# Performance work log

Hardware: AMD Instinct MI355X
Metric: run time of the kernel (lower is better)

Reference implementation:

```python
import jax, jax.numpy as jnp
import numpy as np

B, T, D = 4, 4096, 1024
HD = 64              # head_dim
H = D // HD          # n_heads = 16
C = 64               # chunk_size (T % C == 0)


def setup_inputs() -> dict:
    key = jax.random.key(0)
    k1, k2, k3 = jax.random.split(key, 3)
    out = jax.random.normal(k1, (B, T, D), jnp.float32)
    # Linear(d_model, d_model, bias=False) weights, ~1/sqrt(D) scale
    W_write = jax.random.normal(k2, (D, D), jnp.float32) * 0.03
    W_read = jax.random.normal(k3, (D, D), jnp.float32) * 0.03
    decay = jnp.full((H,), 4.6, jnp.float32)                 # torch init value
    log_alpha = jnp.log(jnp.full((H,), 0.03, jnp.float32))   # memory_alpha=0.03
    return {"out": out, "W_write": W_write, "W_read": W_read,
            "decay": decay, "log_alpha": log_alpha}


def reference(out, W_write, W_read, decay, log_alpha):
    Bb, Tt, Dd = out.shape
    d, Hh, Cc = HD, D // HD, C
    out32 = out.astype(jnp.float32)
    gamma = jax.nn.sigmoid(decay)          # (H,)
    log_gamma = jnp.log(gamma)

    # projections and head split: (B, H, T, d)
    v = (out32 @ W_write.T).reshape(Bb, Tt, Hh, d).transpose(0, 2, 1, 3)
    rk = out32.reshape(Bb, Tt, Hh, d).transpose(0, 2, 1, 3)
    wk = jnp.pad(rk[:, :, :-1], ((0, 0), (0, 0), (1, 0), (0, 0)))  # shift right by 1

    BH = Bb * Hh
    gamma_bh = jnp.tile(gamma, Bb)          # (BH,) index b*H+h -> gamma[h]
    log_gamma_bh = jnp.tile(log_gamma, Bb)
    nC = Tt // Cc
    # (nC, BH, C, d) so lax.scan runs over chunks
    v_ch = v.reshape(BH, nC, Cc, d).transpose(1, 0, 2, 3)
    rk_ch = rk.reshape(BH, nC, Cc, d).transpose(1, 0, 2, 3)
    wk_ch = wk.reshape(BH, nC, Cc, d).transpose(1, 0, 2, 3)

    p = jnp.arange(Cc)
    diffs = jnp.clip(p[:, None] - 1 - p[None, :], 0)          # (C, C)
    causal = p[:, None] > p[None, :]
    # per-(b,h) intra-chunk decay mask (BH, C, C)
    M = jnp.exp(diffs[None].astype(jnp.float32) * log_gamma_bh[:, None, None]) * causal[None]
    g_p = gamma_bh[:, None] ** p[None, :].astype(jnp.float32)            # (BH, C)
    g_w = gamma_bh[:, None] ** (Cc - 1 - p)[None, :].astype(jnp.float32)  # (BH, C)
    g_C = gamma_bh ** Cc                                                  # (BH,)

    def scan_fn(W, chunk):
        rk_c, wk_c, v_c = chunk                                   # each (BH, C, d)
        inter = jnp.einsum('bij,bcj->bci', W, rk_c) * g_p[:, :, None]
        S = jnp.einsum('bcd,bkd->bck', rk_c, wk_c)                # (BH, C, C)
        intra = jnp.einsum('bck,bkd->bcd', S * M, v_c)
        W_new = g_C[:, None, None] * W + jnp.einsum('bci,bcj->bij', v_c * g_w[:, :, None], wk_c)
        return W_new, inter + intra

    W0 = jnp.zeros((BH, d, d), jnp.float32)
    _, reads = jax.lax.scan(scan_fn, W0, (rk_ch, wk_ch, v_ch))   # (nC, BH, C, d)
    reads = reads.transpose(1, 0, 2, 3).reshape(Bb, Hh, Tt, d)
    alpha = jnp.exp(log_alpha)[None, :, None, None]
    reads = (alpha * reads).transpose(0, 2, 1, 3).reshape(Bb, Tt, Dd)
    return out + (reads @ W_read.T).astype(out.dtype)
```

## Files before the change

kernel.cpp:

```cpp
#include <hip/hip_runtime.h>
#include <hip/hip_bf16.h>
#include <stdint.h>


typedef __bf16 bf16x8 __attribute__((ext_vector_type(8)));
typedef float f32x4 __attribute__((ext_vector_type(4)));

#define GAS __attribute__((address_space(1)))
#define LAS __attribute__((address_space(3)))

__device__ __forceinline__ unsigned short f2bf(float f) {
  unsigned u = __float_as_uint(f);
  u = (u + 0x7fffu + ((u >> 16) & 1u)) >> 16;
  return (unsigned short)u;
}
__device__ __forceinline__ float bf2f(unsigned short h) {
  return __uint_as_float(((unsigned)h) << 16);
}

__global__ __launch_bounds__(256) void cast_f32_to_bf16(
    const float* __restrict__ src, unsigned short* __restrict__ dst, int n8) {
  int i = blockIdx.x * 256 + threadIdx.x;
  if (i >= n8) return;
  const float4* s = (const float4*)src + (size_t)i * 2;
  float4 f0 = s[0], f1 = s[1];
  union { uint4 u4; unsigned short us[8]; } o;
  o.us[0] = f2bf(f0.x); o.us[1] = f2bf(f0.y); o.us[2] = f2bf(f0.z); o.us[3] = f2bf(f0.w);
  o.us[4] = f2bf(f1.x); o.us[5] = f2bf(f1.y); o.us[6] = f2bf(f1.z); o.us[7] = f2bf(f1.w);
  ((uint4*)dst)[i] = o.u4;
}

__device__ __forceinline__ void swizzle_bm_bn(int id, int& bm, int& bn) {
  int x = id & 7;
  int s = id >> 3;
  bn = s & 7;
  bm = ((s >> 3) << 3) | x;
}

__global__ __launch_bounds__(256, 4) void gemm_bt_bf16out(
    const unsigned short* __restrict__ A, const unsigned short* __restrict__ B,
    unsigned short* __restrict__ C, int M, int N, int K) {
  __shared__ unsigned short As[2][128 * 32];
  __shared__ unsigned short Bs[2][128 * 32];
  int tid = threadIdx.x;
  int l = tid & 63, w = tid >> 6;
  int bm, bn;
  swizzle_bm_bn(blockIdx.x, bm, bn);
  int wm = (w >> 1) * 64, wn = (w & 1) * 64;
  f32x4 acc[4][4];
#pragma unroll
  for (int mi = 0; mi < 4; mi++)
#pragma unroll
    for (int ni = 0; ni < 4; ni++) acc[mi][ni] = (f32x4){0.f, 0.f, 0.f, 0.f};
  const unsigned short* Ab = A + (size_t)bm * 128 * K;
  const unsigned short* Bb = B + (size_t)bn * 128 * K;
  int lr = l >> 2, lc = (l & 3) * 8;
  int lm = l & 15, q4 = l >> 4;
  const int nit = K >> 5;

#pragma unroll
  for (int q = 0; q < 2; q++) {
    int g = (w * 2 + q) * 16 + lr;
    __builtin_amdgcn_global_load_lds((GAS void*)(void*)(Ab + (size_t)g * K + lc),
                                     (LAS void*)(&As[0][(w * 2 + q) * 512]), 16, 0, 0);
    __builtin_amdgcn_global_load_lds((GAS void*)(void*)(Bb + (size_t)g * K + lc),
                                     (LAS void*)(&Bs[0][(w * 2 + q) * 512]), 16, 0, 0);
  }
  for (int it = 0; it < nit; it++) {
    __syncthreads();
    int buf = it & 1;
    if (it + 1 < nit) {
      int k0 = (it + 1) << 5;
#pragma unroll
      for (int q = 0; q < 2; q++) {
        int g = (w * 2 + q) * 16 + lr;
        __builtin_amdgcn_global_load_lds((GAS void*)(void*)(Ab + (size_t)g * K + k0 + lc),
                                         (LAS void*)(&As[buf ^ 1][(w * 2 + q) * 512]), 16, 0, 0);
        __builtin_amdgcn_global_load_lds((GAS void*)(void*)(Bb + (size_t)g * K + k0 + lc),
                                         (LAS void*)(&Bs[buf ^ 1][(w * 2 + q) * 512]), 16, 0, 0);
      }
    }
    bf16x8 a[4], b[4];
#pragma unroll
    for (int mi = 0; mi < 4; mi++) a[mi] = *(const bf16x8*)&As[buf][(wm + mi * 16 + lm) * 32 + q4 * 8];
#pragma unroll
    for (int ni = 0; ni < 4; ni++) b[ni] = *(const bf16x8*)&Bs[buf][(wn + ni * 16 + lm) * 32 + q4 * 8];
#pragma unroll
    for (int mi = 0; mi < 4; mi++)
#pragma unroll
      for (int ni = 0; ni < 4; ni++)
        acc[mi][ni] = __builtin_amdgcn_mfma_f32_16x16x32_bf16(a[mi], b[ni], acc[mi][ni], 0, 0, 0);
  }
#pragma unroll
  for (int mi = 0; mi < 4; mi++)
#pragma unroll
    for (int ni = 0; ni < 4; ni++) {
      int r0 = bm * 128 + wm + mi * 16 + q4 * 4;
      int col = bn * 128 + wn + ni * 16 + lm;
#pragma unroll
      for (int j = 0; j < 4; j++)
        C[(size_t)(r0 + j) * N + col] = f2bf(acc[mi][ni][j]);
    }
}

__global__ __launch_bounds__(256, 4) void gemm_bt_addout(
    const unsigned short* __restrict__ A, const unsigned short* __restrict__ B,
    const float* __restrict__ base, float* __restrict__ C, int M, int N, int K) {
  __shared__ unsigned short As[2][128 * 32];
  __shared__ unsigned short Bs[2][128 * 32];
  int tid = threadIdx.x;
  int l = tid & 63, w = tid >> 6;
  int bm, bn;
  swizzle_bm_bn(blockIdx.x, bm, bn);
  int wm = (w >> 1) * 64, wn = (w & 1) * 64;
  int lr = l >> 2, lc = (l & 3) * 8;
  int lm = l & 15, q4 = l >> 4;
  f32x4 acc[4][4];
#pragma unroll
  for (int mi = 0; mi < 4; mi++)
#pragma unroll
    for (int ni = 0; ni < 4; ni++) {
      int r0 = bm * 128 + wm + mi * 16 + q4 * 4;
      int col = bn * 128 + wn + ni * 16 + lm;
#pragma unroll
      for (int j = 0; j < 4; j++)
        acc[mi][ni][j] = base[(size_t)(r0 + j) * N + col];
    }
  const unsigned short* Ab = A + (size_t)bm * 128 * K;
  const unsigned short* Bb = B + (size_t)bn * 128 * K;
  const int nit = K >> 5;
#pragma unroll
  for (int q = 0; q < 2; q++) {
    int g = (w * 2 + q) * 16 + lr;
    __builtin_amdgcn_global_load_lds((GAS void*)(void*)(Ab + (size_t)g * K + lc),
                                     (LAS void*)(&As[0][(w * 2 + q) * 512]), 16, 0, 0);
    __builtin_amdgcn_global_load_lds((GAS void*)(void*)(Bb + (size_t)g * K + lc),
                                     (LAS void*)(&Bs[0][(w * 2 + q) * 512]), 16, 0, 0);
  }
  for (int it = 0; it < nit; it++) {
    __syncthreads();
    int buf = it & 1;
    if (it + 1 < nit) {
      int k0 = (it + 1) << 5;
#pragma unroll
      for (int q = 0; q < 2; q++) {
        int g = (w * 2 + q) * 16 + lr;
        __builtin_amdgcn_global_load_lds((GAS void*)(void*)(Ab + (size_t)g * K + k0 + lc),
                                         (LAS void*)(&As[buf ^ 1][(w * 2 + q) * 512]), 16, 0, 0);
        __builtin_amdgcn_global_load_lds((GAS void*)(void*)(Bb + (size_t)g * K + k0 + lc),
                                         (LAS void*)(&Bs[buf ^ 1][(w * 2 + q) * 512]), 16, 0, 0);
      }
    }
    bf16x8 a[4], b[4];
#pragma unroll
    for (int mi = 0; mi < 4; mi++) a[mi] = *(const bf16x8*)&As[buf][(wm + mi * 16 + lm) * 32 + q4 * 8];
#pragma unroll
    for (int ni = 0; ni < 4; ni++) b[ni] = *(const bf16x8*)&Bs[buf][(wn + ni * 16 + lm) * 32 + q4 * 8];
#pragma unroll
    for (int mi = 0; mi < 4; mi++)
#pragma unroll
      for (int ni = 0; ni < 4; ni++)
        acc[mi][ni] = __builtin_amdgcn_mfma_f32_16x16x32_bf16(a[mi], b[ni], acc[mi][ni], 0, 0, 0);
  }
#pragma unroll
  for (int mi = 0; mi < 4; mi++)
#pragma unroll
    for (int ni = 0; ni < 4; ni++) {
      int r0 = bm * 128 + wm + mi * 16 + q4 * 4;
      int col = bn * 128 + wn + ni * 16 + lm;
#pragma unroll
      for (int j = 0; j < 4; j++)
        C[(size_t)(r0 + j) * N + col] = acc[mi][ni][j];
    }
}

__global__ __launch_bounds__(256) void chunk_local(
    const unsigned short* __restrict__ rkg,
    const unsigned short* __restrict__ vg,
    const float* __restrict__ decay,
    unsigned short* __restrict__ intra_bf,
    unsigned short* __restrict__ U_bf) {
  int c = blockIdx.x, bh = blockIdx.y;
  int b = bh >> 4, h = bh & 15;
  int tid = threadIdx.x, l = tid & 63, w = tid >> 6;
  float gamma = 1.0f / (1.0f + __expf(-decay[h]));
  float lg = __logf(gamma);

  __shared__ unsigned short rk_s[64 * 72];
  __shared__ unsigned short wk_s[64 * 72];
  __shared__ unsigned short wkT_s[64 * 72];
  __shared__ unsigned short vT_s[64 * 72];
  __shared__ unsigned short S_s[64 * 72];

  const size_t rowbase = (((size_t)b * 4096 + (size_t)c * 64) * 1024) + h * 64;

#pragma unroll
  for (int r = 0; r < 2; r++) {
    int e = r * 256 + tid;
    int p = e >> 3, seg = e & 7;
    uint4 dr = *(const uint4*)(rkg + rowbase + (size_t)p * 1024 + seg * 8);
    *(uint4*)&rk_s[p * 72 + seg * 8] = dr;
    uint4 dv = *(const uint4*)(vg + rowbase + (size_t)p * 1024 + seg * 8);
    {
      unsigned uu[4] = {dv.x, dv.y, dv.z, dv.w};
#pragma unroll
      for (int qq = 0; qq < 4; qq++) {
        vT_s[(seg * 8 + qq * 2) * 72 + p] = (unsigned short)(uu[qq] & 0xffffu);
        vT_s[(seg * 8 + qq * 2 + 1) * 72 + p] = (unsigned short)(uu[qq] >> 16);
      }
    }
    int tg = c * 64 + p - 1;
    uint4 dw = make_uint4(0u, 0u, 0u, 0u);
    if (tg >= 0) dw = *(const uint4*)(rkg + ((size_t)b * 4096 + tg) * 1024 + h * 64 + seg * 8);
    *(uint4*)&wk_s[p * 72 + seg * 8] = dw;
    {
      unsigned uu[4] = {dw.x, dw.y, dw.z, dw.w};
#pragma unroll
      for (int qq = 0; qq < 4; qq++) {
        wkT_s[(seg * 8 + qq * 2) * 72 + p] = (unsigned short)(uu[qq] & 0xffffu);
        wkT_s[(seg * 8 + qq * 2 + 1) * 72 + p] = (unsigned short)(uu[qq] >> 16);
      }
    }
  }
  __syncthreads();

  int lm = l & 15, q4 = l >> 4;

  {
    bf16x8 a0 = *(const bf16x8*)&rk_s[(w * 16 + lm) * 72 + q4 * 8];
    bf16x8 a1 = *(const bf16x8*)&rk_s[(w * 16 + lm) * 72 + 32 + q4 * 8];
#pragma unroll
    for (int ni = 0; ni < 4; ni++) {
      bf16x8 b0 = *(const bf16x8*)&wk_s[(ni * 16 + lm) * 72 + q4 * 8];
      bf16x8 b1 = *(const bf16x8*)&wk_s[(ni * 16 + lm) * 72 + 32 + q4 * 8];
      f32x4 acc = {0.f, 0.f, 0.f, 0.f};
      acc = __builtin_amdgcn_mfma_f32_16x16x32_bf16(a0, b0, acc, 0, 0, 0);
      acc = __builtin_amdgcn_mfma_f32_16x16x32_bf16(a1, b1, acc, 0, 0, 0);
#pragma unroll
      for (int j = 0; j < 4; j++) {
        int p = w * 16 + q4 * 4 + j;
        int q = ni * 16 + lm;
        float m = (p > q) ? __expf(lg * (float)(p - 1 - q)) : 0.0f;
        S_s[p * 72 + q] = f2bf(acc[j] * m);
      }
    }
  }
  __syncthreads();

  {
    bf16x8 a0 = *(const bf16x8*)&S_s[(w * 16 + lm) * 72 + q4 * 8];
    bf16x8 a1 = *(const bf16x8*)&S_s[(w * 16 + lm) * 72 + 32 + q4 * 8];
#pragma unroll
    for (int ni = 0; ni < 4; ni++) {
      bf16x8 b0 = *(const bf16x8*)&vT_s[(ni * 16 + lm) * 72 + q4 * 8];
      bf16x8 b1 = *(const bf16x8*)&vT_s[(ni * 16 + lm) * 72 + 32 + q4 * 8];
      f32x4 acc = {0.f, 0.f, 0.f, 0.f};
      acc = __builtin_amdgcn_mfma_f32_16x16x32_bf16(a0, b0, acc, 0, 0, 0);
      acc = __builtin_amdgcn_mfma_f32_16x16x32_bf16(a1, b1, acc, 0, 0, 0);
#pragma unroll
      for (int j = 0; j < 4; j++) {
        int p = w * 16 + q4 * 4 + j;
        int i = ni * 16 + lm;
        intra_bf[rowbase + (size_t)p * 1024 + i] = f2bf(acc[j]);
      }
    }
  }

  {
    bf16x8 a0 = *(const bf16x8*)&vT_s[(w * 16 + lm) * 72 + q4 * 8];
    bf16x8 a1 = *(const bf16x8*)&vT_s[(w * 16 + lm) * 72 + 32 + q4 * 8];
#pragma unroll
    for (int jj = 0; jj < 8; jj++) {
      int p0 = q4 * 8 + jj;
      a0[jj] = (__bf16)((float)a0[jj] * __expf(lg * (float)(63 - p0)));
      a1[jj] = (__bf16)((float)a1[jj] * __expf(lg * (float)(63 - (p0 + 32))));
    }
    size_t ub = ((size_t)bh * 64 + c) * 4096;
#pragma unroll
    for (int nj = 0; nj < 4; nj++) {
      bf16x8 b0 = *(const bf16x8*)&wkT_s[(nj * 16 + lm) * 72 + q4 * 8];
      bf16x8 b1 = *(const bf16x8*)&wkT_s[(nj * 16 + lm) * 72 + 32 + q4 * 8];
      f32x4 acc = {0.f, 0.f, 0.f, 0.f};
      acc = __builtin_amdgcn_mfma_f32_16x16x32_bf16(a0, b0, acc, 0, 0, 0);
      acc = __builtin_amdgcn_mfma_f32_16x16x32_bf16(a1, b1, acc, 0, 0, 0);
#pragma unroll
      for (int j = 0; j < 4; j++) {
        int i = w * 16 + q4 * 4 + j;
        int col = nj * 16 + lm;
        U_bf[ub + i * 64 + col] = f2bf(acc[j]);
      }
    }
  }
}

__global__ __launch_bounds__(256) void scan_matmul(
    const unsigned short* __restrict__ U_bf, unsigned short* __restrict__ Wst,
    const float* __restrict__ decay) {
  int col0 = blockIdx.x * 128, bh = blockIdx.y, h = bh & 15;
  int tid = threadIdx.x, l = tid & 63, w = tid >> 6;
  float gamma = 1.0f / (1.0f + __expf(-decay[h]));
  float lgC = 64.0f * __logf(gamma);

  __shared__ unsigned short L_s[64 * 72];
  __shared__ unsigned short B_s[128 * 72];

  {
    int m = tid >> 2, kk0 = (tid & 3) * 16;
#pragma unroll
    for (int e = 0; e < 16; e++) {
      int k = kk0 + e;
      float v = (k < m) ? __expf(lgC * (float)(m - 1 - k)) : 0.0f;
      L_s[m * 72 + k] = f2bf(v);
    }
  }
  size_t ub = (size_t)bh * 64 * 4096 + col0;
#pragma unroll
  for (int it = 0; it < 4; it++) {
    int e = it * 256 + tid;
    int k = e >> 4, seg = e & 15;
    uint4 d = *(const uint4*)(U_bf + ub + (size_t)k * 4096 + seg * 8);
    unsigned uu[4] = {d.x, d.y, d.z, d.w};
#pragma unroll
    for (int qq = 0; qq < 4; qq++) {
      B_s[(seg * 8 + qq * 2) * 72 + k] = (unsigned short)(uu[qq] & 0xffffu);
      B_s[(seg * 8 + qq * 2 + 1) * 72 + k] = (unsigned short)(uu[qq] >> 16);
    }
  }
  __syncthreads();

  int lm = l & 15, q4 = l >> 4;
  f32x4 acc[4][2];
#pragma unroll
  for (int mi = 0; mi < 4; mi++)
#pragma unroll
    for (int ni = 0; ni < 2; ni++) acc[mi][ni] = (f32x4){0.f, 0.f, 0.f, 0.f};
#pragma unroll
  for (int kk = 0; kk < 2; kk++) {
    bf16x8 a[4], b[2];
#pragma unroll
    for (int mi = 0; mi < 4; mi++)
      a[mi] = *(const bf16x8*)&L_s[(mi * 16 + lm) * 72 + kk * 32 + q4 * 8];
#pragma unroll
    for (int ni = 0; ni < 2; ni++)
      b[ni] = *(const bf16x8*)&B_s[(w * 32 + ni * 16 + lm) * 72 + kk * 32 + q4 * 8];
#pragma unroll
    for (int mi = 0; mi < 4; mi++)
#pragma unroll
      for (int ni = 0; ni < 2; ni++)
        acc[mi][ni] = __builtin_amdgcn_mfma_f32_16x16x32_bf16(a[mi], b[ni], acc[mi][ni], 0, 0, 0);
  }
  size_t wb = (size_t)bh * 64 * 4096 + col0;
#pragma unroll
  for (int mi = 0; mi < 4; mi++)
#pragma unroll
    for (int ni = 0; ni < 2; ni++)
#pragma unroll
      for (int j = 0; j < 4; j++) {
        int c = mi * 16 + q4 * 4 + j;
        int n = w * 32 + ni * 16 + lm;
        Wst[wb + (size_t)c * 4096 + n] = f2bf(acc[mi][ni][j]);
      }
}

__global__ __launch_bounds__(256) void inter_combine(
    const unsigned short* __restrict__ rkg, const unsigned short* __restrict__ Wst,
    const unsigned short* __restrict__ intra_bf,
    const float* __restrict__ decay, const float* __restrict__ log_alpha,
    unsigned short* __restrict__ reads_bf) {
  int c = blockIdx.x, bh = blockIdx.y;
  int b = bh >> 4, h = bh & 15;
  int tid = threadIdx.x, l = tid & 63, w = tid >> 6;
  float gamma = 1.0f / (1.0f + __expf(-decay[h]));
  float lg = __logf(gamma);
  float alpha = __expf(log_alpha[h]);
  __shared__ unsigned short rk_s[64 * 72];
  __shared__ unsigned short W_s[64 * 72];
  const size_t rowbase = (((size_t)b * 4096 + (size_t)c * 64) * 1024) + h * 64;
  size_t wbase = ((size_t)bh * 64 + c) * 4096;
#pragma unroll
  for (int r = 0; r < 2; r++) {
    int e = r * 256 + tid;
    int p = e >> 3, seg = e & 7;
    *(uint4*)&rk_s[p * 72 + seg * 8] = *(const uint4*)(rkg + rowbase + (size_t)p * 1024 + seg * 8);
    *(uint4*)&W_s[p * 72 + seg * 8] = *(const uint4*)(Wst + wbase + (size_t)e * 8);
  }
  __syncthreads();
  int lm = l & 15, q4 = l >> 4;
  bf16x8 a0 = *(const bf16x8*)&rk_s[(w * 16 + lm) * 72 + q4 * 8];
  bf16x8 a1 = *(const bf16x8*)&rk_s[(w * 16 + lm) * 72 + 32 + q4 * 8];
#pragma unroll
  for (int ni = 0; ni < 4; ni++) {
    bf16x8 b0 = *(const bf16x8*)&W_s[(ni * 16 + lm) * 72 + q4 * 8];
    bf16x8 b1 = *(const bf16x8*)&W_s[(ni * 16 + lm) * 72 + 32 + q4 * 8];
    f32x4 acc = {0.f, 0.f, 0.f, 0.f};
    acc = __builtin_amdgcn_mfma_f32_16x16x32_bf16(a0, b0, acc, 0, 0, 0);
    acc = __builtin_amdgcn_mfma_f32_16x16x32_bf16(a1, b1, acc, 0, 0, 0);
#pragma unroll
    for (int j = 0; j < 4; j++) {
      int p = w * 16 + q4 * 4 + j;
      int i = ni * 16 + lm;
      float gp = __expf(lg * (float)p);
      size_t ad = rowbase + (size_t)p * 1024 + i;
      reads_bf[ad] = f2bf(alpha * (acc[j] * gp + bf2f(intra_bf[ad])));
    }
  }
}

extern "C" void kernel_launch(void* const* d_in, const int* in_sizes, int n_in,
                              void* d_out, int out_size, void* d_ws, size_t ws_size,
                              hipStream_t stream) {
  const float* out_f = (const float*)d_in[0];
  const float* Ww = (const float*)d_in[1];
  const float* Wr = (const float*)d_in[2];
  const float* decay = (const float*)d_in[3];
  const float* lalpha = (const float*)d_in[4];

  char* ws = (char*)d_ws;
  unsigned short* outbf = (unsigned short*)(ws + 0);
  unsigned short* vbf   = (unsigned short*)(ws + 33554432);
  unsigned short* wwbf  = (unsigned short*)(ws + 67108864);
  unsigned short* wrbf  = (unsigned short*)(ws + 69206016);
  unsigned short* intra = (unsigned short*)(ws + 71303168);
  unsigned short* U     = (unsigned short*)(ws + 104857600);
  unsigned short* Wst   = (unsigned short*)(ws + 138412032);
  unsigned short* reads = (unsigned short*)(ws + 171966464);

  cast_f32_to_bf16<<<dim3(8192), 256, 0, stream>>>(out_f, outbf, 16777216 / 8);
  cast_f32_to_bf16<<<dim3(512), 256, 0, stream>>>(Ww, wwbf, 1048576 / 8);
  cast_f32_to_bf16<<<dim3(512), 256, 0, stream>>>(Wr, wrbf, 1048576 / 8);

  gemm_bt_bf16out<<<dim3(1024), 256, 0, stream>>>(outbf, wwbf, vbf, 16384, 1024, 1024);

  chunk_local<<<dim3(64, 64), 256, 0, stream>>>(outbf, vbf, decay, intra, U);
  scan_matmul<<<dim3(32, 64), 256, 0, stream>>>(U, Wst, decay);
  inter_combine<<<dim3(64, 64), 256, 0, stream>>>(outbf, Wst, intra, decay, lalpha, reads);

  gemm_bt_addout<<<dim3(1024), 256, 0, stream>>>(reads, wrbf, out_f, (float*)d_out,
                                                 16384, 1024, 1024);
}
```

Before: 298.4 us.

## Fuse chunk-state scan with inter-chunk read and use bf16 residual

```diff
diff --git a/kernel.cpp b/kernel.cpp
--- a/kernel.cpp
+++ b/kernel.cpp
@@ -23,6 +23,20 @@
   int i = blockIdx.x * 256 + threadIdx.x;
   if (i >= n8) return;
   const float4* s = (const float4*)src + (size_t)i * 2;
+  float4 f0 = s[0], f1 = s[1];
+  union { uint4 u4; unsigned short us[8]; } o;
+  o.us[0] = f2bf(f0.x); o.us[1] = f2bf(f0.y); o.us[2] = f2bf(f0.z); o.us[3] = f2bf(f0.w);
+  o.us[4] = f2bf(f1.x); o.us[5] = f2bf(f1.y); o.us[6] = f2bf(f1.z); o.us[7] = f2bf(f1.w);
+  ((uint4*)dst)[i] = o.u4;
+}
+
+__global__ __launch_bounds__(256) void cast_weights(
+    const float* __restrict__ w1, const float* __restrict__ w2,
+    unsigned short* __restrict__ dst) {
+  int i = blockIdx.x * 256 + threadIdx.x;
+  const float* src = (i < 131072) ? w1 : w2;
+  int j = (i < 131072) ? i : i - 131072;
+  const float4* s = (const float4*)src + (size_t)j * 2;
   float4 f0 = s[0], f1 = s[1];
   union { uint4 u4; unsigned short us[8]; } o;
   o.us[0] = f2bf(f0.x); o.us[1] = f2bf(f0.y); o.us[2] = f2bf(f0.z); o.us[3] = f2bf(f0.w);
@@ -57,7 +71,6 @@
   int lr = l >> 2, lc = (l & 3) * 8;
   int lm = l & 15, q4 = l >> 4;
   const int nit = K >> 5;
-
 #pragma unroll
   for (int q = 0; q < 2; q++) {
     int g = (w * 2 + q) * 16 + lr;
@@ -105,7 +118,7 @@
 
 __global__ __launch_bounds__(256, 4) void gemm_bt_addout(
     const unsigned short* __restrict__ A, const unsigned short* __restrict__ B,
-    const float* __restrict__ base, float* __restrict__ C, int M, int N, int K) {
+    const unsigned short* __restrict__ base_bf, float* __restrict__ C, int M, int N, int K) {
   __shared__ unsigned short As[2][128 * 32];
   __shared__ unsigned short Bs[2][128 * 32];
   int tid = threadIdx.x;
@@ -124,7 +137,7 @@
       int col = bn * 128 + wn + ni * 16 + lm;
 #pragma unroll
       for (int j = 0; j < 4; j++)
-        acc[mi][ni][j] = base[(size_t)(r0 + j) * N + col];
+        acc[mi][ni][j] = bf2f(base_bf[(size_t)(r0 + j) * N + col]);
     }
   const unsigned short* Ab = A + (size_t)bm * 128 * K;
   const unsigned short* Bb = B + (size_t)bn * 128 * K;
@@ -293,116 +306,72 @@
   }
 }
 
-__global__ __launch_bounds__(256) void scan_matmul(
-    const unsigned short* __restrict__ U_bf, unsigned short* __restrict__ Wst,
-    const float* __restrict__ decay) {
-  int col0 = blockIdx.x * 128, bh = blockIdx.y, h = bh & 15;
-  int tid = threadIdx.x, l = tid & 63, w = tid >> 6;
-  float gamma = 1.0f / (1.0f + __expf(-decay[h]));
-  float lgC = 64.0f * __logf(gamma);
-
-  __shared__ unsigned short L_s[64 * 72];
-  __shared__ unsigned short B_s[128 * 72];
-
-  {
-    int m = tid >> 2, kk0 = (tid & 3) * 16;
-#pragma unroll
-    for (int e = 0; e < 16; e++) {
-      int k = kk0 + e;
-      float v = (k < m) ? __expf(lgC * (float)(m - 1 - k)) : 0.0f;
-      L_s[m * 72 + k] = f2bf(v);
-    }
-  }
-  size_t ub = (size_t)bh * 64 * 4096 + col0;
-#pragma unroll
-  for (int it = 0; it < 4; it++) {
-    int e = it * 256 + tid;
-    int k = e >> 4, seg = e & 15;
-    uint4 d = *(const uint4*)(U_bf + ub + (size_t)k * 4096 + seg * 8);
-    unsigned uu[4] = {d.x, d.y, d.z, d.w};
-#pragma unroll
-    for (int qq = 0; qq < 4; qq++) {
-      B_s[(seg * 8 + qq * 2) * 72 + k] = (unsigned short)(uu[qq] & 0xffffu);
-      B_s[(seg * 8 + qq * 2 + 1) * 72 + k] = (unsigned short)(uu[qq] >> 16);
-    }
-  }
-  __syncthreads();
-
-  int lm = l & 15, q4 = l >> 4;
-  f32x4 acc[4][2];
-#pragma unroll
-  for (int mi = 0; mi < 4; mi++)
-#pragma unroll
-    for (int ni = 0; ni < 2; ni++) acc[mi][ni] = (f32x4){0.f, 0.f, 0.f, 0.f};
-#pragma unroll
-  for (int kk = 0; kk < 2; kk++) {
-    bf16x8 a[4], b[2];
-#pragma unroll
-    for (int mi = 0; mi < 4; mi++)
-      a[mi] = *(const bf16x8*)&L_s[(mi * 16 + lm) * 72 + kk * 32 + q4 * 8];
-#pragma unroll
-    for (int ni = 0; ni < 2; ni++)
-      b[ni] = *(const bf16x8*)&B_s[(w * 32 + ni * 16 + lm) * 72 + kk * 32 + q4 * 8];
-#pragma unroll
-    for (int mi = 0; mi < 4; mi++)
-#pragma unroll
-      for (int ni = 0; ni < 2; ni++)
-        acc[mi][ni] = __builtin_amdgcn_mfma_f32_16x16x32_bf16(a[mi], b[ni], acc[mi][ni], 0, 0, 0);
-  }
-  size_t wb = (size_t)bh * 64 * 4096 + col0;
-#pragma unroll
-  for (int mi = 0; mi < 4; mi++)
-#pragma unroll
-    for (int ni = 0; ni < 2; ni++)
-#pragma unroll
-      for (int j = 0; j < 4; j++) {
-        int c = mi * 16 + q4 * 4 + j;
-        int n = w * 32 + ni * 16 + lm;
-        Wst[wb + (size_t)c * 4096 + n] = f2bf(acc[mi][ni][j]);
-      }
-}
-
-__global__ __launch_bounds__(256) void inter_combine(
-    const unsigned short* __restrict__ rkg, const unsigned short* __restrict__ Wst,
+__global__ __launch_bounds__(256) void scan_inter(
+    const unsigned short* __restrict__ rkg, const unsigned short* __restrict__ U_bf,
     const unsigned short* __restrict__ intra_bf,
     const float* __restrict__ decay, const float* __restrict__ log_alpha,
     unsigned short* __restrict__ reads_bf) {
-  int c = blockIdx.x, bh = blockIdx.y;
+  int sp = blockIdx.x, bh = blockIdx.y;
   int b = bh >> 4, h = bh & 15;
   int tid = threadIdx.x, l = tid & 63, w = tid >> 6;
+  int lm = l & 15, q4 = l >> 4;
   float gamma = 1.0f / (1.0f + __expf(-decay[h]));
   float lg = __logf(gamma);
+  float gC = __expf(64.0f * lg);
   float alpha = __expf(log_alpha[h]);
+  int i0 = sp * 16;
+
   __shared__ unsigned short rk_s[64 * 72];
-  __shared__ unsigned short W_s[64 * 72];
-  const size_t rowbase = (((size_t)b * 4096 + (size_t)c * 64) * 1024) + h * 64;
-  size_t wbase = ((size_t)bh * 64 + c) * 4096;
-#pragma unroll
-  for (int r = 0; r < 2; r++) {
-    int e = r * 256 + tid;
-    int p = e >> 3, seg = e & 7;
-    *(uint4*)&rk_s[p * 72 + seg * 8] = *(const uint4*)(rkg + rowbase + (size_t)p * 1024 + seg * 8);
-    *(uint4*)&W_s[p * 72 + seg * 8] = *(const uint4*)(Wst + wbase + (size_t)e * 8);
-  }
-  __syncthreads();
-  int lm = l & 15, q4 = l >> 4;
-  bf16x8 a0 = *(const bf16x8*)&rk_s[(w * 16 + lm) * 72 + q4 * 8];
-  bf16x8 a1 = *(const bf16x8*)&rk_s[(w * 16 + lm) * 72 + 32 + q4 * 8];
-#pragma unroll
-  for (int ni = 0; ni < 4; ni++) {
-    bf16x8 b0 = *(const bf16x8*)&W_s[(ni * 16 + lm) * 72 + q4 * 8];
-    bf16x8 b1 = *(const bf16x8*)&W_s[(ni * 16 + lm) * 72 + 32 + q4 * 8];
+  __shared__ unsigned short W_s[16 * 72];
+
+  int lrow = tid >> 4, colb = (tid & 15) * 4;
+  float Wreg[4] = {0.f, 0.f, 0.f, 0.f};
+
+  int p_a = tid >> 3, seg_a = (tid & 7) * 8;
+  const size_t bbase = (size_t)b * 4096 * 1024 + h * 64;
+  size_t ubase = (size_t)bh * 64 * 4096;
+
+  uint4 nrk0 = *(const uint4*)(rkg + bbase + (size_t)p_a * 1024 + seg_a);
+  uint4 nrk1 = *(const uint4*)(rkg + bbase + (size_t)(p_a + 32) * 1024 + seg_a);
+  ushort4 nu = *(const ushort4*)(U_bf + ubase + (i0 + lrow) * 64 + colb);
+
+  for (int c = 0; c < 64; c++) {
+    uint4 rk0 = nrk0, rk1 = nrk1;
+    ushort4 uc = nu;
+    __syncthreads();
+    *(uint4*)&rk_s[p_a * 72 + seg_a] = rk0;
+    *(uint4*)&rk_s[(p_a + 32) * 72 + seg_a] = rk1;
+    {
+      ushort4 wv;
+      wv.x = f2bf(Wreg[0]); wv.y = f2bf(Wreg[1]); wv.z = f2bf(Wreg[2]); wv.w = f2bf(Wreg[3]);
+      *(ushort4*)&W_s[lrow * 72 + colb] = wv;
+    }
+    __syncthreads();
+    if (c + 1 < 64) {
+      size_t nrb = bbase + (size_t)(c + 1) * 64 * 1024;
+      nrk0 = *(const uint4*)(rkg + nrb + (size_t)p_a * 1024 + seg_a);
+      nrk1 = *(const uint4*)(rkg + nrb + (size_t)(p_a + 32) * 1024 + seg_a);
+      nu = *(const ushort4*)(U_bf + ubase + (size_t)(c + 1) * 4096 + (i0 + lrow) * 64 + colb);
+    }
     f32x4 acc = {0.f, 0.f, 0.f, 0.f};
-    acc = __builtin_amdgcn_mfma_f32_16x16x32_bf16(a0, b0, acc, 0, 0, 0);
-    acc = __builtin_amdgcn_mfma_f32_16x16x32_bf16(a1, b1, acc, 0, 0, 0);
+#pragma unroll
+    for (int kst = 0; kst < 2; kst++) {
+      bf16x8 a = *(const bf16x8*)&rk_s[(w * 16 + lm) * 72 + kst * 32 + q4 * 8];
+      bf16x8 bb = *(const bf16x8*)&W_s[lm * 72 + kst * 32 + q4 * 8];
+      acc = __builtin_amdgcn_mfma_f32_16x16x32_bf16(a, bb, acc, 0, 0, 0);
+    }
+    size_t rowbase = bbase + (size_t)c * 64 * 1024;
 #pragma unroll
     for (int j = 0; j < 4; j++) {
-      int p = w * 16 + q4 * 4 + j;
-      int i = ni * 16 + lm;
-      float gp = __expf(lg * (float)p);
-      size_t ad = rowbase + (size_t)p * 1024 + i;
+      int ptok = w * 16 + q4 * 4 + j;
+      float gp = __expf(lg * (float)ptok);
+      size_t ad = rowbase + (size_t)ptok * 1024 + i0 + lm;
       reads_bf[ad] = f2bf(alpha * (acc[j] * gp + bf2f(intra_bf[ad])));
     }
+    Wreg[0] = gC * Wreg[0] + bf2f(uc.x);
+    Wreg[1] = gC * Wreg[1] + bf2f(uc.y);
+    Wreg[2] = gC * Wreg[2] + bf2f(uc.z);
+    Wreg[3] = gC * Wreg[3] + bf2f(uc.w);
   }
 }
 
@@ -422,19 +391,16 @@
   unsigned short* wrbf  = (unsigned short*)(ws + 69206016);
   unsigned short* intra = (unsigned short*)(ws + 71303168);
   unsigned short* U     = (unsigned short*)(ws + 104857600);
-  unsigned short* Wst   = (unsigned short*)(ws + 138412032);
   unsigned short* reads = (unsigned short*)(ws + 171966464);
 
   cast_f32_to_bf16<<<dim3(8192), 256, 0, stream>>>(out_f, outbf, 16777216 / 8);
-  cast_f32_to_bf16<<<dim3(512), 256, 0, stream>>>(Ww, wwbf, 1048576 / 8);
-  cast_f32_to_bf16<<<dim3(512), 256, 0, stream>>>(Wr, wrbf, 1048576 / 8);
+  cast_weights<<<dim3(1024), 256, 0, stream>>>(Ww, Wr, wwbf);
 
   gemm_bt_bf16out<<<dim3(1024), 256, 0, stream>>>(outbf, wwbf, vbf, 16384, 1024, 1024);
 
   chunk_local<<<dim3(64, 64), 256, 0, stream>>>(outbf, vbf, decay, intra, U);
-  scan_matmul<<<dim3(32, 64), 256, 0, stream>>>(U, Wst, decay);
-  inter_combine<<<dim3(64, 64), 256, 0, stream>>>(outbf, Wst, intra, decay, lalpha, reads);
-
-  gemm_bt_addout<<<dim3(1024), 256, 0, stream>>>(reads, wrbf, out_f, (float*)d_out,
+  scan_inter<<<dim3(4, 64), 256, 0, stream>>>(outbf, U, intra, decay, lalpha, reads);
+
+  gemm_bt_addout<<<dim3(1024), 256, 0, stream>>>(reads, wrbf, outbf, (float*)d_out,
                                                  16384, 1024, 1024);
 }
```

Measured after the change: 297.5 us. No clear change (-0.3%).
